# Kernel optimization log

Measured on AMD Instinct MI355X. Metric: run time of the kernel, lower is better.

## Reference

```python
import math
import jax, jax.numpy as jnp
import numpy as np

EMBD_DIM = 1024
N_HEADS = 16
WINDOW = 9           # odd, per assert
STRIDE = WINDOW // 2 # 4
BS, T = 4, 4096      # t % stride == 0


def setup_inputs() -> dict:
    key = jax.random.key(0)
    ks = jax.random.split(key, 8)
    c = EMBD_DIM
    std = 0.02
    inp = {
        "q": jax.random.normal(ks[0], (BS, c, T), dtype=jnp.float32),
        "q_mask": jnp.ones((BS, 1, T), dtype=bool),
        # 1x1 Conv1d projections == pointwise linear: W (out, in), b (out,)
        "Wq": jax.random.normal(ks[1], (c, c), dtype=jnp.float32) * std,
        "bq": jnp.zeros((c,), dtype=jnp.float32),
        "Wk": jax.random.normal(ks[2], (c, c), dtype=jnp.float32) * std,
        "bk": jnp.zeros((c,), dtype=jnp.float32),
        "Wv": jax.random.normal(ks[3], (c, c), dtype=jnp.float32) * std,
        "bv": jnp.zeros((c,), dtype=jnp.float32),
        "Wp": jax.random.normal(ks[4], (c, c), dtype=jnp.float32) * std,
        "bp": jnp.zeros((c,), dtype=jnp.float32),
    }
    return inp


def _pointwise(x, W, b):
    # 1x1 Conv1d on (bs, c, t)
    return jnp.einsum('oc,bct->bot', W, x) + b[None, :, None]


def reference(q, q_mask, Wq, bq, Wk, bk, Wv, bv, Wp, bp):
    bs, c, t = q.shape
    h, w, s = N_HEADS, WINDOW, STRIDE
    d = c // h
    scale = 1.0 / math.sqrt(d)

    qq = _pointwise(q, Wq, bq)
    kk = _pointwise(q, Wk, bk)  # self-attention: k = v = q
    vv = _pointwise(q, Wv, bv)

    def split_heads(x):  # (bs, c, t) -> (bs*h, t, d)
        return x.reshape(bs, h, d, t).transpose(0, 1, 3, 2).reshape(bs * h, t, d)

    qh = split_heads(qq) * scale
    kh = split_heads(kk)
    vh = split_heads(vv)

    # Sliding-window indices: query i attends to keys j in [i-s, i+s].
    # This is exactly the band produced by the chunked as_strided code plus
    # its l_mask/r_mask boundary fills (which mask j < 0 and j >= t).
    offs = jnp.arange(-s, s + 1)                 # (w,)
    idx = jnp.arange(t)[:, None] + offs[None, :] # (t, w)
    in_range = (idx >= 0) & (idx < t)
    idxc = jnp.clip(idx, 0, t - 1)

    k_win = kh[:, idxc]                          # (bs*h, t, w, d)
    scores = jnp.einsum('ntd,ntwd->ntw', qh, k_win)
    scores = scores.reshape(bs, h, t, w)

    # kv mask: invalid key positions contribute -10000 (as in _attn_normalize)
    kv_valid = q_mask.reshape(bs, t)
    kv_bias = jnp.where(kv_valid[:, idxc], 0.0, -10000.0)  # (bs, t, w)
    scores = scores + kv_bias[:, None]
    scores = jnp.where(in_range[None, None], scores, -jnp.inf)

    attn = jax.nn.softmax(scores, axis=-1)
    # zero attention rows at invalid query positions
    attn = jnp.where(kv_valid[:, None, :, None], attn, 0.0)
    attn = attn.reshape(bs * h, t, w)

    v_win = vh[:, idxc]                          # (bs*h, t, w, d)
    out = jnp.einsum('ntw,ntwd->ntd', attn, v_win)

    out = out.reshape(bs, h, t, d).transpose(0, 1, 3, 2).reshape(bs, c, t)
    out = _pointwise(out, Wp, bp) * q_mask.astype(out.dtype)
    return (out, q_mask)
```

## Files before the change

### kernel.cpp

```cpp
#include <hip/hip_runtime.h>
#include <hip/hip_bf16.h>
#include <math.h>

#define T_SEQ 4096
#define C_DIM 1024
#define NH    16
#define HD    64
#define BSZ   4
#define VSTRIDE 4120
#define VPAD    12

typedef __attribute__((ext_vector_type(8))) short bf16x8;
typedef __attribute__((ext_vector_type(4))) float f32x4;

__device__ __forceinline__ unsigned short f2bf(float f) {
    union { __hip_bfloat16 h; unsigned short u; } cv;
    cv.h = __float2bfloat16(f);
    return cv.u;
}

__global__ __launch_bounds__(256) void conv_w_kernel(
    const float* __restrict__ Wq, const float* __restrict__ Wk,
    const float* __restrict__ Wv, const float* __restrict__ Wp,
    __hip_bfloat16* __restrict__ Wqkv, __hip_bfloat16* __restrict__ Wpb,
    const int* __restrict__ mask, float* __restrict__ mout)
{
    int bid = blockIdx.x;
    if (bid >= 4096) {
        int i = (bid - 4096) * 256 + threadIdx.x;
        if (i < BSZ * T_SEQ) mout[i] = (mask[i] != 0) ? 1.0f : 0.0f;
        return;
    }
    int i = bid * 256 + threadIdx.x;
    int which = i >> 18;
    int off = (i & 262143) << 2;
    const float* src = which == 0 ? Wq : which == 1 ? Wk : which == 2 ? Wv : Wp;
    float4 v = *reinterpret_cast<const float4*>(src + off);
    ushort4 o;
    o.x = f2bf(v.x); o.y = f2bf(v.y); o.z = f2bf(v.z); o.w = f2bf(v.w);
    __hip_bfloat16* dst = (which < 3) ? (Wqkv + ((size_t)which << 20) + off) : (Wpb + off);
    *reinterpret_cast<ushort4*>(dst) = o;
}

__global__ __launch_bounds__(256) void transpose_x_kernel(
    const float* __restrict__ q, __hip_bfloat16* __restrict__ xT)
{
    __shared__ float tile[64][65];
    int t0 = blockIdx.x * 64;
    int c0 = blockIdx.y * 64;
    int b  = blockIdx.z;
    int tx = threadIdx.x & 63;
    int ty = threadIdx.x >> 6;
    const float* src = q + ((size_t)b * C_DIM + c0) * T_SEQ + t0;
    #pragma unroll
    for (int i = 0; i < 16; ++i) {
        int c = ty + i * 4;
        tile[c][tx] = src[(size_t)c * T_SEQ + tx];
    }
    __syncthreads();
    __hip_bfloat16* dst = xT + ((size_t)b * T_SEQ + t0) * C_DIM + c0;
    #pragma unroll
    for (int i = 0; i < 16; ++i) {
        int t = ty + i * 4;
        dst[(size_t)t * C_DIM + tx] = __float2bfloat16(tile[tx][t]);
    }
}

__device__ __forceinline__ void stage_slot(
    const __hip_bfloat16* __restrict__ Ab, const __hip_bfloat16* __restrict__ Bb,
    __hip_bfloat16* As, __hip_bfloat16* Bs, int kbase, int tid, int wid)
{
    #pragma unroll
    for (int i = 0; i < 2; ++i) {
        int c = i * 512 + tid;
        int r = c >> 2;
        int sg = (c & 3) ^ ((r >> 1) & 3);
        const __hip_bfloat16* src = Ab + (size_t)r * C_DIM + kbase + sg * 8;
        __builtin_amdgcn_global_load_lds(
            (const __attribute__((address_space(1))) void*)src,
            (__attribute__((address_space(3))) void*)(As + (i * 512 + wid * 64) * 8),
            16, 0, 0);
    }
    {
        int c = tid;
        int r = c >> 2;
        int sg = (c & 3) ^ ((r >> 1) & 3);
        const __hip_bfloat16* src = Bb + (size_t)r * C_DIM + kbase + sg * 8;
        __builtin_amdgcn_global_load_lds(
            (const __attribute__((address_space(1))) void*)src,
            (__attribute__((address_space(3))) void*)(Bs + (wid * 64) * 8),
            16, 0, 0);
    }
}

#define GEMM_PIPELINE_CORE()                                                         \
    f32x4 acc[4][4] = {};                                                            \
    stage_slot(Abase, Bbase, Alds + 0 * 8192, Blds + 0 * 4096, 0, tid, wid);         \
    stage_slot(Abase, Bbase, Alds + 1 * 8192, Blds + 1 * 4096, 32, tid, wid);        \
    const int NST = C_DIM / 32;                                                      \
    int cs = 0;                                                                      \
    for (int st = 0; st < NST; ++st) {                                               \
        if (st == NST - 1)                                                           \
            asm volatile("s_waitcnt vmcnt(0)" ::: "memory");                         \
        else                                                                         \
            asm volatile("s_waitcnt vmcnt(3)" ::: "memory");                         \
        __builtin_amdgcn_s_barrier();                                                \
        if (st + 2 < NST) {                                                          \
            int ns = cs + 2; if (ns >= 3) ns -= 3;                                   \
            stage_slot(Abase, Bbase, Alds + ns * 8192, Blds + ns * 4096,             \
                       (st + 2) * 32, tid, wid);                                     \
        }                                                                            \
        const __hip_bfloat16* As = Alds + cs * 8192;                                 \
        const __hip_bfloat16* Bs = Blds + cs * 4096;                                 \
        bf16x8 af[4], bfr[4];                                                        \
        _Pragma("unroll")                                                            \
        for (int mi = 0; mi < 4; ++mi)                                               \
            af[mi] = *reinterpret_cast<const bf16x8*>(                               \
                As + (wr * 64 + mi * 16 + fr) * 32 + sof);                           \
        _Pragma("unroll")                                                            \
        for (int ni = 0; ni < 4; ++ni)                                               \
            bfr[ni] = *reinterpret_cast<const bf16x8*>(                              \
                Bs + (wc * 64 + ni * 16 + fr) * 32 + sof);                           \
        __builtin_amdgcn_s_setprio(1);                                               \
        _Pragma("unroll")                                                            \
        for (int mi = 0; mi < 4; ++mi) {                                             \
            _Pragma("unroll")                                                        \
            for (int ni = 0; ni < 4; ++ni)                                           \
                acc[mi][ni] = __builtin_amdgcn_mfma_f32_16x16x32_bf16(               \
                    af[mi], bfr[ni], acc[mi][ni], 0, 0, 0);                          \
        }                                                                            \
        __builtin_amdgcn_s_setprio(0);                                               \
        cs = cs + 1; if (cs == 3) cs = 0;                                            \
    }

__global__ __launch_bounds__(512, 4) void gemm_qkv_kernel(
    const __hip_bfloat16* __restrict__ A,
    const __hip_bfloat16* __restrict__ xT,
    const float* __restrict__ bq, const float* __restrict__ bk, const float* __restrict__ bv,
    __hip_bfloat16* __restrict__ qh, __hip_bfloat16* __restrict__ kh,
    __hip_bfloat16* __restrict__ vhT)
{
    __shared__ __align__(16) __hip_bfloat16 Sall[36864];
    __hip_bfloat16* Alds = Sall;
    __hip_bfloat16* Blds = Sall + 24576;
    int tid  = threadIdx.x;
    int lane = tid & 63;
    int wid  = tid >> 6;
    int wr = wid >> 1;
    int wc = wid & 1;
    int fr = lane & 15;
    int g  = lane >> 4;
    int sof = (g ^ ((fr >> 1) & 3)) * 8;

    const int NWG = 1536;
    int wg  = blockIdx.x;
    int swz = (wg & 7) * (NWG >> 3) + (wg >> 3);
    int n_i = swz & 31;
    int g2  = swz >> 5;
    int m_i = g2 % 12;
    int b   = g2 / 12;
    int n0 = n_i * 128;
    int m0 = m_i * 256;
    const __hip_bfloat16* Abase = A + (size_t)m0 * C_DIM;
    const __hip_bfloat16* Bbase = xT + ((size_t)b * T_SEQ + n0) * C_DIM;

    GEMM_PIPELINE_CORE()

    __hip_bfloat16* W = Sall + wid * 4608;
    int mrow0 = m0 + wr * 64;
    int which = mrow0 >> 10;
    int o0 = mrow0 & 1023;
    int hh = o0 >> 6;
    int tb = n0 + wc * 64;

    if (which != 2) {
        const float* bias = (which == 0) ? bq : bk;
        __hip_bfloat16* outp = (which == 0) ? qh : kh;
        #pragma unroll
        for (int mi = 0; mi < 4; ++mi) {
            int db = mi * 16 + g * 4;
            float b0 = bias[o0 + db], b1 = bias[o0 + db + 1];
            float b2 = bias[o0 + db + 2], b3 = bias[o0 + db + 3];
            #pragma unroll
            for (int ni = 0; ni < 4; ++ni) {
                ushort4 pk;
                pk.x = f2bf(acc[mi][ni][0] + b0);
                pk.y = f2bf(acc[mi][ni][1] + b1);
                pk.z = f2bf(acc[mi][ni][2] + b2);
                pk.w = f2bf(acc[mi][ni][3] + b3);
                *reinterpret_cast<ushort4*>(W + (ni * 16 + fr) * 72 + db) = pk;
            }
        }
        size_t hb = ((size_t)b * NH + hh) * T_SEQ;
        #pragma unroll
        for (int p = 0; p < 8; ++p) {
            int row = p * 8 + (lane >> 3);
            int ch  = lane & 7;
            bf16x8 v = *reinterpret_cast<const bf16x8*>(W + row * 72 + ch * 8);
            *reinterpret_cast<bf16x8*>(outp + (hb + tb + row) * HD + ch * 8) = v;
        }
    } else {
        #pragma unroll
        for (int mi = 0; mi < 4; ++mi) {
            int db = mi * 16 + g * 4;
            float b0 = bv[o0 + db], b1 = bv[o0 + db + 1];
            float b2 = bv[o0 + db + 2], b3 = bv[o0 + db + 3];
            #pragma unroll
            for (int ni = 0; ni < 4; ++ni) {
                int tl = ni * 16 + fr;
                W[(db + 0) * 72 + tl] = __float2bfloat16(acc[mi][ni][0] + b0);
                W[(db + 1) * 72 + tl] = __float2bfloat16(acc[mi][ni][1] + b1);
                W[(db + 2) * 72 + tl] = __float2bfloat16(acc[mi][ni][2] + b2);
                W[(db + 3) * 72 + tl] = __float2bfloat16(acc[mi][ni][3] + b3);
            }
        }
        size_t rowdb = ((size_t)b * NH + hh) * HD;
        #pragma unroll
        for (int p = 0; p < 8; ++p) {
            int row = p * 8 + (lane >> 3);
            int ch  = lane & 7;
            bf16x8 v = *reinterpret_cast<const bf16x8*>(W + row * 72 + ch * 8);
            ushort4 lo, hi;
            lo.x = (unsigned short)v[0]; lo.y = (unsigned short)v[1];
            lo.z = (unsigned short)v[2]; lo.w = (unsigned short)v[3];
            hi.x = (unsigned short)v[4]; hi.y = (unsigned short)v[5];
            hi.z = (unsigned short)v[6]; hi.w = (unsigned short)v[7];
            __hip_bfloat16* dst = vhT + (rowdb + row) * VSTRIDE + VPAD + tb + ch * 8;
            *reinterpret_cast<ushort4*>(dst)     = lo;
            *reinterpret_cast<ushort4*>(dst + 4) = hi;
        }
    }
}

__global__ __launch_bounds__(512, 4) void gemm_proj_kernel(
    const __hip_bfloat16* __restrict__ A,
    const __hip_bfloat16* __restrict__ xT,
    const float* __restrict__ bp,
    const int* __restrict__ mask,
    float* __restrict__ out)
{
    __shared__ __align__(16) __hip_bfloat16 Sall[36864];
    __hip_bfloat16* Alds = Sall;
    __hip_bfloat16* Blds = Sall + 24576;
    int tid  = threadIdx.x;
    int lane = tid & 63;
    int wid  = tid >> 6;
    int wr = wid >> 1;
    int wc = wid & 1;
    int fr = lane & 15;
    int g  = lane >> 4;
    int sof = (g ^ ((fr >> 1) & 3)) * 8;

    int wg  = blockIdx.x;
    int swz = (wg & 7) * 64 + (wg >> 3);
    int n_i = swz & 31;
    int g2  = swz >> 5;
    int m_i = g2 & 3;
    int b   = g2 >> 2;
    int n0 = n_i * 128;
    int m0 = m_i * 256;
    const __hip_bfloat16* Abase = A + (size_t)m0 * C_DIM;
    const __hip_bfloat16* Bbase = xT + ((size_t)b * T_SEQ + n0) * C_DIM;

    GEMM_PIPELINE_CORE()

    float* Wf = reinterpret_cast<float*>(Sall) + wid * 2176;
    int tb = n0 + wc * 64;
    const int* mrow = mask + b * T_SEQ + tb;

    #pragma unroll
    for (int pass = 0; pass < 2; ++pass) {
        #pragma unroll
        for (int mi2 = 0; mi2 < 2; ++mi2) {
            int mi = pass * 2 + mi2;
            int db = mi * 16 + g * 4;
            int rr = mi2 * 16 + g * 4;
            int orow = m0 + wr * 64 + db;
            float b0 = bp[orow], b1 = bp[orow + 1], b2 = bp[orow + 2], b3 = bp[orow + 3];
            #pragma unroll
            for (int ni = 0; ni < 4; ++ni) {
                int tl = ni * 16 + fr;
                float mval = (mrow[tl] != 0) ? 1.0f : 0.0f;
                Wf[(rr + 0) * 68 + tl] = (acc[mi][ni][0] + b0) * mval;
                Wf[(rr + 1) * 68 + tl] = (acc[mi][ni][1] + b1) * mval;
                Wf[(rr + 2) * 68 + tl] = (acc[mi][ni][2] + b2) * mval;
                Wf[(rr + 3) * 68 + tl] = (acc[mi][ni][3] + b3) * mval;
            }
        }
        #pragma unroll
        for (int p = 0; p < 8; ++p) {
            int row = p * 4 + (lane >> 4);
            int c4  = lane & 15;
            float4 v = *reinterpret_cast<const float4*>(Wf + row * 68 + c4 * 4);
            int orow = m0 + wr * 64 + pass * 32 + row;
            *reinterpret_cast<float4*>(
                out + ((size_t)b * C_DIM + orow) * T_SEQ + tb + c4 * 4) = v;
        }
    }
}

__global__ __launch_bounds__(256) void attn_kernel(
    const __hip_bfloat16* __restrict__ qh,
    const __hip_bfloat16* __restrict__ kh,
    const __hip_bfloat16* __restrict__ vhT,
    const int* __restrict__ mask,
    __hip_bfloat16* __restrict__ attnT)
{
    __shared__ __hip_bfloat16 Plds[4][16 * 40];
    int lane = threadIdx.x & 63;
    int wid  = threadIdx.x >> 6;
    int gw = blockIdx.x * 4 + wid;
    int bh = gw >> 7;
    int tg = gw & 127;
    int b = bh >> 4, h = bh & 15;
    size_t kqbase = (size_t)bh * T_SEQ * HD;
    const int* mrow = mask + b * T_SEQ;
    int fr = lane & 15;
    int g  = lane >> 4;
    char* pby = (char*)(&Plds[wid][0]);
    f32x4 zacc = {};

    int t0b = tg * 32;
    bf16x8 kA0[2], kA1[2];
    {
        int kr0 = max(t0b - 4 + fr, 0);
        int kr1 = t0b + 12 + fr;
        #pragma unroll
        for (int ks = 0; ks < 2; ++ks) {
            kA0[ks] = *reinterpret_cast<const bf16x8*>(kh + kqbase + (size_t)kr0 * HD + ks * 32 + g * 8);
            kA1[ks] = *reinterpret_cast<const bf16x8*>(kh + kqbase + (size_t)kr1 * HD + ks * 32 + g * 8);
        }
    }

    #pragma unroll
    for (int it = 0; it < 2; ++it) {
        int t0 = t0b + it * 16;
        if (it == 1) {
            #pragma unroll
            for (int ks = 0; ks < 2; ++ks) kA0[ks] = kA1[ks];
            int kr1 = min(t0 + 12 + fr, T_SEQ - 1);
            #pragma unroll
            for (int ks = 0; ks < 2; ++ks)
                kA1[ks] = *reinterpret_cast<const bf16x8*>(kh + kqbase + (size_t)kr1 * HD + ks * 32 + g * 8);
        }
        bf16x8 qB[2];
        #pragma unroll
        for (int ks = 0; ks < 2; ++ks)
            qB[ks] = *reinterpret_cast<const bf16x8*>(qh + kqbase + (size_t)(t0 + fr) * HD + ks * 32 + g * 8);

        f32x4 sacc[2] = {zacc, zacc};
        #pragma unroll
        for (int ks = 0; ks < 2; ++ks) {
            sacc[0] = __builtin_amdgcn_mfma_f32_16x16x32_bf16(kA0[ks], qB[ks], sacc[0], 0, 0, 0);
            sacc[1] = __builtin_amdgcn_mfma_f32_16x16x32_bf16(kA1[ks], qB[ks], sacc[1], 0, 0, 0);
        }

        float ev[2][4];
        float ss = 0.0f;
        #pragma unroll
        for (int mt = 0; mt < 2; ++mt) {
            #pragma unroll
            for (int r = 0; r < 4; ++r) {
                int j = mt * 16 + g * 4 + r;
                int jg = t0 - 4 + j;
                int w = j - fr;
                int jc = min(max(jg, 0), T_SEQ - 1);
                float sv = sacc[mt][r] * 0.125f + (mrow[jc] != 0 ? 0.0f : -10000.0f);
                bool valid = (w >= 0) && (w <= 8) && (jg >= 0) && (jg < T_SEQ);
                float e2 = valid ? __expf(sv) : 0.0f;
                ev[mt][r] = e2;
                ss += e2;
            }
        }
        ss += __shfl_xor(ss, 16);
        ss += __shfl_xor(ss, 32);
        float inv = 1.0f / ss;

        #pragma unroll
        for (int mt = 0; mt < 2; ++mt) {
            unsigned int lo = (unsigned int)f2bf(ev[mt][0] * inv) | ((unsigned int)f2bf(ev[mt][1] * inv) << 16);
            unsigned int hi = (unsigned int)f2bf(ev[mt][2] * inv) | ((unsigned int)f2bf(ev[mt][3] * inv) << 16);
            int jb = (mt * 16 + g * 4) * 2;
            *reinterpret_cast<unsigned int*>(pby + fr * 80 + jb)     = lo;
            *reinterpret_cast<unsigned int*>(pby + fr * 80 + jb + 4) = hi;
        }
        bf16x8 pB = *reinterpret_cast<const bf16x8*>(pby + fr * 80 + g * 16);

        int t = t0 + fr;
        float mq = (mrow[t] != 0) ? 1.0f : 0.0f;
        #pragma unroll
        for (int dt = 0; dt < 4; ++dt) {
            bf16x8 vA = *reinterpret_cast<const bf16x8*>(
                vhT + ((size_t)bh * HD + dt * 16 + fr) * VSTRIDE + VPAD + (t0 - 4) + g * 8);
            f32x4 o = __builtin_amdgcn_mfma_f32_16x16x32_bf16(vA, pB, zacc, 0, 0, 0);
            ushort4 pk;
            pk.x = f2bf(o[0] * mq);
            pk.y = f2bf(o[1] * mq);
            pk.z = f2bf(o[2] * mq);
            pk.w = f2bf(o[3] * mq);
            *reinterpret_cast<ushort4*>(attnT + ((size_t)b * T_SEQ + t) * C_DIM + h * HD + dt * 16 + g * 4) = pk;
        }
    }
}

extern "C" void kernel_launch(void* const* d_in, const int* in_sizes, int n_in,
                              void* d_out, int out_size, void* d_ws, size_t ws_size,
                              hipStream_t stream)
{
    const float* q     = (const float*)d_in[0];
    const int*   qmask = (const int*)d_in[1];
    const float* Wq    = (const float*)d_in[2];
    const float* bq    = (const float*)d_in[3];
    const float* Wk    = (const float*)d_in[4];
    const float* bk    = (const float*)d_in[5];
    const float* Wv    = (const float*)d_in[6];
    const float* bv    = (const float*)d_in[7];
    const float* Wp    = (const float*)d_in[8];
    const float* bp    = (const float*)d_in[9];
    float* out = (float*)d_out;

    char* ws = (char*)d_ws;
    __hip_bfloat16* Wqkv  = (__hip_bfloat16*)(ws);
    __hip_bfloat16* Wpb   = (__hip_bfloat16*)(ws + 6291456);
    __hip_bfloat16* xT    = (__hip_bfloat16*)(ws + 8388608);
    __hip_bfloat16* attnT = (__hip_bfloat16*)(ws + 8388608);
    __hip_bfloat16* qh    = (__hip_bfloat16*)(ws + 41943040);
    __hip_bfloat16* kh    = (__hip_bfloat16*)(ws + 75497472);
    __hip_bfloat16* vhT   = (__hip_bfloat16*)(ws + 109051904);

    float* mecho = out + (size_t)BSZ * C_DIM * T_SEQ;
    conv_w_kernel<<<4160, 256, 0, stream>>>(Wq, Wk, Wv, Wp, Wqkv, Wpb, qmask, mecho);
    transpose_x_kernel<<<dim3(64, 16, 4), 256, 0, stream>>>(q, xT);
    gemm_qkv_kernel<<<1536, 512, 0, stream>>>(Wqkv, xT, bq, bk, bv, qh, kh, vhT);
    attn_kernel<<<2048, 256, 0, stream>>>(qh, kh, vhT, qmask, attnT);
    gemm_proj_kernel<<<512, 512, 0, stream>>>(Wpb, attnT, bp, qmask, out);
}
```

Baseline: 213.6 us.

## Load B fragments directly to registers and deepen A LDS pipeline to four slots

The GEMM pipeline stops staging the B operand through LDS. Each wave now loads its B fragments straight from global memory into double-buffered registers one step ahead. The A operand pipeline grows from three to four LDS slots with a prefetch distance of three, and the loop is fully unrolled. The aim is to cut LDS traffic and ds_read latency for B and to hide more global latency, at the cost of more VGPRs and redundant global loads of B across the waves that share a column. The new layout uses 32768 bf16 elements of the 36864-element shared buffer.

Result: slower. 385.0 us (+80.3%).

```diff
diff --git a/kernel.cpp b/kernel.cpp
--- a/kernel.cpp
+++ b/kernel.cpp
@@ -66,9 +66,9 @@
     }
 }
 
-__device__ __forceinline__ void stage_slot(
-    const __hip_bfloat16* __restrict__ Ab, const __hip_bfloat16* __restrict__ Bb,
-    __hip_bfloat16* As, __hip_bfloat16* Bs, int kbase, int tid, int wid)
+__device__ __forceinline__ void stage_A(
+    const __hip_bfloat16* __restrict__ Ab,
+    __hip_bfloat16* As, int kbase, int tid, int wid)
 {
     #pragma unroll
     for (int i = 0; i < 2; ++i) {
@@ -81,57 +81,65 @@
             (__attribute__((address_space(3))) void*)(As + (i * 512 + wid * 64) * 8),
             16, 0, 0);
     }
-    {
-        int c = tid;
-        int r = c >> 2;
-        int sg = (c & 3) ^ ((r >> 1) & 3);
-        const __hip_bfloat16* src = Bb + (size_t)r * C_DIM + kbase + sg * 8;
-        __builtin_amdgcn_global_load_lds(
-            (const __attribute__((address_space(1))) void*)src,
-            (__attribute__((address_space(3))) void*)(Bs + (wid * 64) * 8),
-            16, 0, 0);
-    }
 }
 
 #define GEMM_PIPELINE_CORE()                                                         \
     f32x4 acc[4][4] = {};                                                            \
-    stage_slot(Abase, Bbase, Alds + 0 * 8192, Blds + 0 * 4096, 0, tid, wid);         \
-    stage_slot(Abase, Bbase, Alds + 1 * 8192, Blds + 1 * 4096, 32, tid, wid);        \
+    const __hip_bfloat16* Br0 = Bbase + (size_t)(wc * 64 + fr) * C_DIM + g * 8;      \
+    const __hip_bfloat16* Br1 = Br0 + 16 * C_DIM;                                    \
+    const __hip_bfloat16* Br2 = Br0 + 32 * C_DIM;                                    \
+    const __hip_bfloat16* Br3 = Br0 + 48 * C_DIM;                                    \
+    bf16x8 bEv[4], bOd[4];                                                           \
+    bEv[0] = *reinterpret_cast<const bf16x8*>(Br0);                                  \
+    bEv[1] = *reinterpret_cast<const bf16x8*>(Br1);                                  \
+    bEv[2] = *reinterpret_cast<const bf16x8*>(Br2);                                  \
+    bEv[3] = *reinterpret_cast<const bf16x8*>(Br3);                                  \
+    stage_A(Abase, Alds + 0 * 8192, 0, tid, wid);                                    \
+    stage_A(Abase, Alds + 1 * 8192, 32, tid, wid);                                   \
+    stage_A(Abase, Alds + 2 * 8192, 64, tid, wid);                                   \
     const int NST = C_DIM / 32;                                                      \
-    int cs = 0;                                                                      \
+    _Pragma("unroll")                                                                \
     for (int st = 0; st < NST; ++st) {                                               \
-        if (st == NST - 1)                                                           \
+        if (st == 0)                                                                 \
+            asm volatile("s_waitcnt vmcnt(4)" ::: "memory");                         \
+        else if (st <= NST - 3)                                                      \
+            asm volatile("s_waitcnt vmcnt(2)" ::: "memory");                         \
+        else                                                                         \
             asm volatile("s_waitcnt vmcnt(0)" ::: "memory");                         \
-        else                                                                         \
-            asm volatile("s_waitcnt vmcnt(3)" ::: "memory");                         \
         __builtin_amdgcn_s_barrier();                                                \
-        if (st + 2 < NST) {                                                          \
-            int ns = cs + 2; if (ns >= 3) ns -= 3;                                   \
-            stage_slot(Abase, Bbase, Alds + ns * 8192, Blds + ns * 4096,             \
-                       (st + 2) * 32, tid, wid);                                     \
+        if (st + 1 < NST) {                                                          \
+            int kn = (st + 1) * 32;                                                  \
+            if ((st & 1) == 0) {                                                     \
+                bOd[0] = *reinterpret_cast<const bf16x8*>(Br0 + kn);                 \
+                bOd[1] = *reinterpret_cast<const bf16x8*>(Br1 + kn);                 \
+                bOd[2] = *reinterpret_cast<const bf16x8*>(Br2 + kn);                 \
+                bOd[3] = *reinterpret_cast<const bf16x8*>(Br3 + kn);                 \
+            } else {                                                                 \
+                bEv[0] = *reinterpret_cast<const bf16x8*>(Br0 + kn);                 \
+                bEv[1] = *reinterpret_cast<const bf16x8*>(Br1 + kn);                 \
+                bEv[2] = *reinterpret_cast<const bf16x8*>(Br2 + kn);                 \
+                bEv[3] = *reinterpret_cast<const bf16x8*>(Br3 + kn);                 \
+            }                                                                        \
         }                                                                            \
-        const __hip_bfloat16* As = Alds + cs * 8192;                                 \
-        const __hip_bfloat16* Bs = Blds + cs * 4096;                                 \
-        bf16x8 af[4], bfr[4];                                                        \
+        if (st + 3 < NST)                                                            \
+            stage_A(Abase, Alds + ((st + 3) & 3) * 8192, (st + 3) * 32, tid, wid);   \
+        const __hip_bfloat16* As = Alds + (st & 3) * 8192;                           \
+        bf16x8 af[4];                                                                \
         _Pragma("unroll")                                                            \
         for (int mi = 0; mi < 4; ++mi)                                               \
             af[mi] = *reinterpret_cast<const bf16x8*>(                               \
                 As + (wr * 64 + mi * 16 + fr) * 32 + sof);                           \
-        _Pragma("unroll")                                                            \
-        for (int ni = 0; ni < 4; ++ni)                                               \
-            bfr[ni] = *reinterpret_cast<const bf16x8*>(                              \
-                Bs + (wc * 64 + ni * 16 + fr) * 32 + sof);                           \
         __builtin_amdgcn_s_setprio(1);                                               \
         _Pragma("unroll")                                                            \
         for (int mi = 0; mi < 4; ++mi) {                                             \
             _Pragma("unroll")                                                        \
             for (int ni = 0; ni < 4; ++ni)                                           \
                 acc[mi][ni] = __builtin_amdgcn_mfma_f32_16x16x32_bf16(               \
-                    af[mi], bfr[ni], acc[mi][ni], 0, 0, 0);                          \
+                    af[mi], ((st & 1) ? bOd[ni] : bEv[ni]), acc[mi][ni], 0, 0, 0);   \
         }                                                                            \
         __builtin_amdgcn_s_setprio(0);                                               \
-        cs = cs + 1; if (cs == 3) cs = 0;                                            \
-    }
+    }                                                                                \
+    __syncthreads();
 
 __global__ __launch_bounds__(512, 4) void gemm_qkv_kernel(
     const __hip_bfloat16* __restrict__ A,
@@ -142,7 +150,6 @@
 {
     __shared__ __align__(16) __hip_bfloat16 Sall[36864];
     __hip_bfloat16* Alds = Sall;
-    __hip_bfloat16* Blds = Sall + 24576;
     int tid  = threadIdx.x;
     int lane = tid & 63;
     int wid  = tid >> 6;
@@ -241,7 +248,6 @@
 {
     __shared__ __align__(16) __hip_bfloat16 Sall[36864];
     __hip_bfloat16* Alds = Sall;
-    __hip_bfloat16* Blds = Sall + 24576;
     int tid  = threadIdx.x;
     int lane = tid & 63;
     int wid  = tid >> 6;
```
